# Kernel optimization log

Hardware: AMD Instinct MI355X
Metric: run time of the kernel (lower is better)

Reference implementation:

```python
import jax, jax.numpy as jnp
import numpy as np

NEG_SLOPE = 0.2  # GATConv default negative_slope


def gat_conv(x, row, col, W, b, a_src, a_dst, N):
    # GATConv, heads=1, flow='target_to_source': i=row (central), j=col (neighbor)
    h = x @ W                                                   # [N, C]
    e = jax.nn.leaky_relu((h @ a_src)[col] + (h @ a_dst)[row], NEG_SLOPE)  # [E]
    m = jax.ops.segment_max(e, row, num_segments=N)             # segment softmax over row
    w = jnp.exp(e - m[row])
    denom = jax.ops.segment_sum(w, row, num_segments=N)
    alpha = w / (denom[row] + 1e-16)
    out = jax.ops.segment_sum(alpha[:, None] * h[col], row, num_segments=N)
    return out + b


def lstm_scan(xs_t, Wih, Whh, bih, bhh):
    # xs_t: [L, N, C] -> hidden states [L, N, H]; PyTorch gate order i,f,g,o
    H = Whh.shape[1]
    Nn = xs_t.shape[1]
    bias = bih + bhh
    def step(carry, xt):
        h, c = carry
        g = xt @ Wih.T + h @ Whh.T + bias
        i, f, gg, o = jnp.split(g, 4, axis=-1)
        c = jax.nn.sigmoid(f) * c + jax.nn.sigmoid(i) * jnp.tanh(gg)
        h = jax.nn.sigmoid(o) * jnp.tanh(c)
        return (h, c), h
    init = (jnp.zeros((Nn, H), xs_t.dtype), jnp.zeros((Nn, H), xs_t.dtype))
    _, hs = jax.lax.scan(step, init, xs_t)
    return hs


def jk_lstm(xst, Wih_f, Whh_f, bih_f, bhh_f, Wih_b, Whh_b, bih_b, bhh_b, att_W, att_b):
    # xst: [L, N, C]; bidirectional LSTM over layer dim, attention-weighted sum
    hf = lstm_scan(xst, Wih_f, Whh_f, bih_f, bhh_f)
    hb = lstm_scan(xst[::-1], Wih_b, Whh_b, bih_b, bhh_b)[::-1]
    h = jnp.concatenate([hf, hb], axis=-1)                      # [L, N, 2H]
    score = jnp.einsum('lnh,h->ln', h, att_W) + att_b           # [L, N]
    alpha = jax.nn.softmax(score, axis=0)                       # softmax over layers
    return jnp.einsum('lnc,ln->nc', xst, alpha)                 # [N, C]


def setup_inputs() -> dict:
    key = jax.random.key(0)
    ks = list(jax.random.split(key, 32))
    N, E, C = 50000, 800000, 128
    L = 3
    H = (L * C) // 2  # 192; PyG JumpingKnowledge lstm hidden size
    s = 0.05
    d = {}
    d['x'] = jax.random.normal(ks[0], (N, 3), jnp.float32)
    d['edge_index'] = jax.random.randint(ks[1], (2, E), 0, N, jnp.int64)
    d['gat_W0'] = jax.random.normal(ks[2], (3, C)) * 0.3
    d['gat_b0'] = jnp.zeros((C,))
    d['gat_as0'] = jax.random.normal(ks[3], (C,)) * s
    d['gat_ad0'] = jax.random.normal(ks[4], (C,)) * s
    d['gat_W'] = jax.random.normal(ks[5], (L - 1, C, C)) * s
    d['gat_b'] = jnp.zeros((L - 1, C))
    d['gat_as'] = jax.random.normal(ks[6], (L - 1, C)) * s
    d['gat_ad'] = jax.random.normal(ks[7], (L - 1, C)) * s
    d['lstm_Wih_f'] = jax.random.normal(ks[8], (4 * H, C)) * s
    d['lstm_Whh_f'] = jax.random.normal(ks[9], (4 * H, H)) * s
    d['lstm_bih_f'] = jnp.zeros((4 * H,))
    d['lstm_bhh_f'] = jnp.zeros((4 * H,))
    d['lstm_Wih_b'] = jax.random.normal(ks[10], (4 * H, C)) * s
    d['lstm_Whh_b'] = jax.random.normal(ks[11], (4 * H, H)) * s
    d['lstm_bih_b'] = jnp.zeros((4 * H,))
    d['lstm_bhh_b'] = jnp.zeros((4 * H,))
    d['att_W'] = jax.random.normal(ks[12], (2 * H,)) * s
    d['att_b'] = jnp.zeros((1,))
    d['nW1'] = jax.random.normal(ks[13], (C, C)) * s
    d['nb1'] = jnp.zeros((C,))
    d['nW2'] = jax.random.normal(ks[14], (C, 2)) * s
    d['nb2'] = jnp.zeros((2,))
    d['eW1'] = jax.random.normal(ks[15], (2 * C, C)) * s
    d['eb1'] = jnp.zeros((C,))
    d['eW2'] = jax.random.normal(ks[16], (C, 2)) * s
    d['eb2'] = jnp.zeros((2,))
    return d


def reference(x, edge_index, gat_W0, gat_b0, gat_as0, gat_ad0, gat_W, gat_b, gat_as, gat_ad,
              lstm_Wih_f, lstm_Whh_f, lstm_bih_f, lstm_bhh_f,
              lstm_Wih_b, lstm_Whh_b, lstm_bih_b, lstm_bhh_b,
              att_W, att_b, nW1, nb1, nW2, nb2, eW1, eb1, eW2, eb2):
    N = x.shape[0]
    row, col = edge_index[0], edge_index[1]
    xs = []
    h = jax.nn.relu(gat_conv(x, row, col, gat_W0, gat_b0, gat_as0, gat_ad0, N))
    xs.append(h)
    for l in range(gat_W.shape[0]):  # fixed small layer count
        h = jax.nn.relu(gat_conv(h, row, col, gat_W[l], gat_b[l], gat_as[l], gat_ad[l], N))
        xs.append(h)
    xst = jnp.stack(xs, axis=0)  # [L, N, C]
    h = jk_lstm(xst, lstm_Wih_f, lstm_Whh_f, lstm_bih_f, lstm_bhh_f,
                lstm_Wih_b, lstm_Whh_b, lstm_bih_b, lstm_bhh_b, att_W, att_b)
    # node classifier (dropout is identity in eval)
    node_out = jax.nn.softmax(jax.nn.relu(h @ nW1 + nb1) @ nW2 + nb2, axis=1)
    # edge representation gather + concat, then edge classifier
    edge_rep = jnp.concatenate([h[row], h[col]], axis=1)  # [E, 2C]
    edge_out = jax.nn.softmax(jax.nn.relu(edge_rep @ eW1 + eb1) @ eW2 + eb2, axis=1)
    return node_out, edge_out
```

## Files before the change

### kernel.cpp

```cpp
#include <hip/hip_runtime.h>
#include <cstdint>
#include <cstddef>


#define NIN 28
#define MAXJOBS 20

struct InPtrs { const void* p[NIN]; int n[NIN]; };

struct ConvJobs {
    const void* src[MAXJOBS];
    float* dst[MAXJOBS];
    int n[MAXJOBS];
    int ai[MAXJOBS];
    int blk0[MAXJOBS + 1];
    int njobs;
};

typedef short s16x4 __attribute__((ext_vector_type(4)));
typedef short s16x8 __attribute__((ext_vector_type(8)));
typedef float f32x4 __attribute__((ext_vector_type(4)));
typedef unsigned short u16x8 __attribute__((ext_vector_type(8)));

__device__ __forceinline__ float bf2f(unsigned short v) {
    unsigned int u = ((unsigned int)v) << 16;
    return __uint_as_float(u);
}

__device__ __forceinline__ unsigned short f2bf(float x) {
    unsigned int u = __float_as_uint(x);
    unsigned int r = u + 0x7fffu + ((u >> 16) & 1u);
    return (unsigned short)(r >> 16);
}

__device__ __forceinline__ float rdx(const void* p, size_t i, int isf32) {
    return isf32 ? ((const float*)p)[i] : bf2f(((const unsigned short*)p)[i]);
}

__device__ __forceinline__ float frcp(float x) {
    return __builtin_amdgcn_rcpf(x);
}

__device__ __forceinline__ float sigm(float x) {
    return frcp(1.f + __expf(-x));
}

__device__ __forceinline__ float fast_tanh(float x) {
    return 1.f - 2.f * frcp(__expf(2.f * x) + 1.f);
}

__global__ void k_sniff(InPtrs in, int* flags) {
    int ai = blockIdx.x;
    if (ai >= NIN) return;
    __shared__ int cnt;
    if (threadIdx.x == 0) cnt = 0;
    __syncthreads();
    if (ai == 1) {
        const int* w = (const int*)in.p[1];
        int nw = in.n[1] < 512 ? in.n[1] : 512;
        int local = 0;
        for (int i = threadIdx.x; i < nw; i += blockDim.x)
            if ((i & 1) && w[i] != 0) local++;
        atomicAdd(&cnt, local);
        __syncthreads();
        if (threadIdx.x == 0) flags[1] = (cnt < 4) ? 1 : 0;
        return;
    }
    const unsigned short* u = (const unsigned short*)in.p[ai];
    int ns = in.n[ai] < 256 ? in.n[ai] : 256;
    int local = 0;
    for (int i = threadIdx.x; i < ns; i += blockDim.x) {
        if (i & 1) continue;
        unsigned short v = u[i];
        int e = (v >> 7) & 0xff;
        if ((v & 0x7fff) != 0 && (e < 100 || e > 154)) local++;
    }
    atomicAdd(&cnt, local);
    __syncthreads();
    if (threadIdx.x == 0) flags[ai] = (cnt * 4 >= ns) ? 1 : 0;
}

__global__ void k_convall(ConvJobs J, const int* __restrict__ flags) {
    int b = blockIdx.x;
    int j = 0;
    while (j + 1 < J.njobs && b >= J.blk0[j + 1]) ++j;
    int i = (b - J.blk0[j]) * 256 + threadIdx.x;
    if (i >= J.n[j]) return;
    J.dst[j][i] = rdx(J.src[j], i, flags[J.ai[j]]);
}

__global__ void k_conve(const void* src, int* row, int* col, int* cnt,
                        int E, const int* flags) {
    int i = blockIdx.x * blockDim.x + threadIdx.x;
    if (i >= E) return;
    int r, c;
    if (flags[1]) {
        const long long* s = (const long long*)src;
        r = (int)s[i];
        c = (int)s[(size_t)E + i];
    } else {
        const int* s = (const int*)src;
        r = s[i];
        c = s[(size_t)E + i];
    }
    row[i] = r;
    col[i] = c;
    atomicAdd(&cnt[r], 1);
}

__global__ void k_scan1(const int* __restrict__ deg, int* __restrict__ indptr,
                        int* __restrict__ bsums, int N) {
    __shared__ int buf[1024];
    const int t = threadIdx.x;
    const int base = blockIdx.x * 1024;
    int v = (base + t < N) ? deg[base + t] : 0;
    buf[t] = v;
    __syncthreads();
    for (int ofs = 1; ofs < 1024; ofs <<= 1) {
        int add = (t >= ofs) ? buf[t - ofs] : 0;
        __syncthreads();
        buf[t] += add;
        __syncthreads();
    }
    if (base + t < N) indptr[base + t] = buf[t] - v;
    if (t == 1023) bsums[blockIdx.x] = buf[1023];
}

__global__ void k_scan2(int* bsums, int nb) {
    if (threadIdx.x == 0 && blockIdx.x == 0) {
        int acc = 0;
        for (int j = 0; j < nb; ++j) { int v = bsums[j]; bsums[j] = acc; acc += v; }
        bsums[nb] = acc;
    }
}

__global__ void k_scan3(const int* __restrict__ bsums, int* __restrict__ indptr,
                        int* __restrict__ cnt, int N, int nb) {
    int i = blockIdx.x * blockDim.x + threadIdx.x;
    if (i < N) {
        indptr[i] += bsums[i >> 10];
        cnt[i] = 0;
    }
    if (i == 0) indptr[N] = bsums[nb];
}

__global__ void k_fill(const int* __restrict__ row, const int* __restrict__ col,
                       const int* __restrict__ indptr, int* __restrict__ cur,
                       int* __restrict__ colS, int* __restrict__ eidx, int E) {
    int i = blockIdx.x * blockDim.x + threadIdx.x;
    if (i >= E) return;
    int r = row[i];
    int p = indptr[r] + atomicAdd(&cur[r], 1);
    colS[p] = col[i];
    eidx[p] = i;
}

__global__ __launch_bounds__(256) void k_lin0(
    const float* __restrict__ x, const float* __restrict__ W0,
    const float* __restrict__ asrc, const float* __restrict__ adst,
    unsigned short* __restrict__ hlin, float* __restrict__ hs, float* __restrict__ hd,
    int N) {
    const int wid = threadIdx.x >> 6, lane = threadIdx.x & 63;
    const int n = blockIdx.x * 4 + wid;
    if (n >= N) return;
    float x0 = x[(size_t)n * 3], x1 = x[(size_t)n * 3 + 1], x2 = x[(size_t)n * 3 + 2];
    const int c0 = lane, c1 = lane + 64;
    float h0 = x0 * W0[c0] + x1 * W0[128 + c0] + x2 * W0[256 + c0];
    float h1 = x0 * W0[c1] + x1 * W0[128 + c1] + x2 * W0[256 + c1];
    hlin[(size_t)n * 128 + c0] = f2bf(h0);
    hlin[(size_t)n * 128 + c1] = f2bf(h1);
    float sp = h0 * asrc[c0] + h1 * asrc[c1];
    float dp = h0 * adst[c0] + h1 * adst[c1];
    for (int o = 32; o; o >>= 1) { sp += __shfl_down(sp, o); dp += __shfl_down(dp, o); }
    if (lane == 0) { hs[n] = sp; hd[n] = dp; }
}

__global__ void k_wpackg(const float* __restrict__ Wcanon,
                         unsigned short* __restrict__ Wg) {
    int idx = blockIdx.x * blockDim.x + threadIdx.x;
    if (idx >= 2 * 4 * 8 * 512) return;
    int layer = idx / 16384;
    int r  = idx % 16384;
    int kb = r / 4096;
    int r2 = r % 4096;
    int f  = r2 / 512;
    int q  = r2 % 512;
    int lane = q >> 3, j = q & 7;
    int k   = kb * 32 + ((j >> 2) * 16) + ((lane >> 4) * 4) + (j & 3);
    int col = f * 16 + (lane & 15);
    Wg[idx] = f2bf(Wcanon[(size_t)layer * 16384 + (size_t)k * 128 + col]);
}

__global__ void k_wpackt(const float* __restrict__ nW1, const float* __restrict__ eW1,
                         unsigned short* __restrict__ Wt) {
    int idx = blockIdx.x * blockDim.x + threadIdx.x;
    if (idx >= 4 * 24 * 512) return;
    int kb = idx / (24 * 512);
    int r  = idx % (24 * 512);
    int fr = r / 512;
    int q  = r % 512;
    int lane = q >> 3, j = q & 7;
    int k   = kb * 32 + ((j >> 2) * 16) + ((lane >> 4) * 4) + (j & 3);
    int grp = fr >> 3;
    int col = (fr & 7) * 16 + (lane & 15);
    float v;
    if (grp == 0)      v = nW1[(size_t)k * 128 + col];
    else if (grp == 1) v = eW1[(size_t)k * 128 + col];
    else               v = eW1[(size_t)(128 + k) * 128 + col];
    Wt[idx] = f2bf(v);
}

__global__ __launch_bounds__(512) void k_linm(
    const unsigned short* __restrict__ xin,
    const unsigned short* __restrict__ Wg,
    const float* __restrict__ asrc, const float* __restrict__ adst,
    unsigned short* __restrict__ hlin, float* __restrict__ hs, float* __restrict__ hd,
    int N) {
    __shared__ unsigned short AS[64][136];
    __shared__ float hsS[64], hdS[64];
    const int t = threadIdx.x;
    const int f = t >> 6, lane = t & 63;
    const int n0 = blockIdx.x * 64;
    const int ccol = lane & 15;
    const int klane = lane >> 4;
    const int lrow = klane * 4;
    const int akl = klane * 4;
    const int m = f * 16 + ccol;

    const float asv = asrc[m], adv = adst[m];

    for (int i = t; i < 1024; i += 512) {
        int r = i >> 4, kq = (i & 15) * 8;
        u16x8 v = (u16x8)(0);
        if (n0 + r < N) v = *(const u16x8*)(xin + (size_t)(n0 + r) * 128 + kq);
        *(u16x8*)&AS[r][kq] = v;
    }
    if (t < 64) { hsS[t] = 0.f; hdS[t] = 0.f; }
    __syncthreads();

    f32x4 acc[4];
    #pragma unroll
    for (int rf = 0; rf < 4; ++rf) acc[rf] = (f32x4)(0.f);
    #pragma unroll
    for (int kb = 0; kb < 4; ++kb) {
        s16x8 b = *(const s16x8*)(Wg + ((size_t)kb * 8 + f) * 512 + lane * 8);
        const int k0 = kb * 32 + akl;
        #pragma unroll
        for (int rf = 0; rf < 4; ++rf) {
            s16x4 alo = *(const s16x4*)&AS[rf * 16 + ccol][k0];
            s16x4 ahi = *(const s16x4*)&AS[rf * 16 + ccol][k0 + 16];
            s16x8 av = __builtin_shufflevector(alo, ahi, 0, 1, 2, 3, 4, 5, 6, 7);
            acc[rf] = __builtin_amdgcn_mfma_f32_16x16x32_bf16(av, b, acc[rf], 0, 0, 0);
        }
    }
    __syncthreads();

    float sp[16], dp[16];
    #pragma unroll
    for (int rf = 0; rf < 4; ++rf) {
        #pragma unroll
        for (int reg = 0; reg < 4; ++reg) {
            float h = acc[rf][reg];
            int ci = rf * 4 + reg;
            AS[rf * 16 + lrow + reg][m] = f2bf(h);
            sp[ci] = h * asv;
            dp[ci] = h * adv;
        }
    }
    #pragma unroll
    for (int o = 1; o < 16; o <<= 1) {
        #pragma unroll
        for (int i = 0; i < 16; ++i) { sp[i] += __shfl_xor(sp[i], o); dp[i] += __shfl_xor(dp[i], o); }
    }
    if (ccol == 0) {
        #pragma unroll
        for (int i = 0; i < 16; ++i) {
            int row = (i >> 2) * 16 + lrow + (i & 3);
            atomicAdd(&hsS[row], sp[i]);
            atomicAdd(&hdS[row], dp[i]);
        }
    }
    __syncthreads();

    for (int i = t; i < 1024; i += 512) {
        int r = i >> 4, kq = (i & 15) * 8;
        if (n0 + r < N)
            *(u16x8*)(hlin + (size_t)(n0 + r) * 128 + kq) = *(const u16x8*)&AS[r][kq];
    }
    if (t < 64 && n0 + t < N) { hs[n0 + t] = hsS[t]; hd[n0 + t] = hdS[t]; }
}

__global__ __launch_bounds__(256) void k_aggr(
    const unsigned short* __restrict__ hlin, const float* __restrict__ hs,
    const float* __restrict__ hd,
    const int* __restrict__ indptr, const int* __restrict__ colS,
    const float* __restrict__ b, unsigned short* __restrict__ xout, int N) {
    const int wid = threadIdx.x >> 6, lane = threadIdx.x & 63;
    const int n = blockIdx.x * 4 + wid;
    if (n >= N) return;
    const int s = indptr[n], epos = indptr[n + 1];
    const float hdv = hd[n];
    const int c0 = lane, c1 = lane + 64;
    float m = -1e30f, d = 0.f, a0 = 0.f, a1 = 0.f;
    int idx = s;
    for (; idx + 8 <= epos; idx += 8) {
        int cl[8];
        #pragma unroll
        for (int j = 0; j < 8; ++j) cl[j] = colS[idx + j];
        float e[8];
        #pragma unroll
        for (int j = 0; j < 8; ++j) {
            float ev = hs[cl[j]] + hdv;
            e[j] = (ev > 0.f) ? ev : 0.2f * ev;
        }
        float v0[8], v1[8];
        #pragma unroll
        for (int j = 0; j < 8; ++j) {
            const unsigned short* hp = hlin + (size_t)cl[j] * 128;
            v0[j] = bf2f(hp[c0]);
            v1[j] = bf2f(hp[c1]);
        }
        float m8 = e[0];
        #pragma unroll
        for (int j = 1; j < 8; ++j) m8 = fmaxf(m8, e[j]);
        if (m8 > m) {
            float sc = __expf(m - m8);
            a0 *= sc; a1 *= sc; d *= sc; m = m8;
        }
        #pragma unroll
        for (int j = 0; j < 8; ++j) {
            float w = __expf(e[j] - m);
            a0 += w * v0[j];
            a1 += w * v1[j];
            d  += w;
        }
    }
    for (; idx < epos; ++idx) {
        int col = colS[idx];
        float e = hs[col] + hdv;
        e = (e > 0.f) ? e : 0.2f * e;
        const unsigned short* hr = hlin + (size_t)col * 128;
        float v0 = bf2f(hr[c0]), v1 = bf2f(hr[c1]);
        if (e > m) {
            float sc = __expf(m - e);
            a0 = a0 * sc + v0;
            a1 = a1 * sc + v1;
            d  = d * sc + 1.f;
            m  = e;
        } else {
            float w = __expf(e - m);
            a0 += w * v0;
            a1 += w * v1;
            d  += w;
        }
    }
    float inv = frcp(d + 1e-16f);
    float r0 = a0 * inv + b[c0];
    float r1 = a1 * inv + b[c1];
    xout[(size_t)n * 128 + c0] = f2bf(fmaxf(r0, 0.f));
    xout[(size_t)n * 128 + c1] = f2bf(fmaxf(r1, 0.f));
}

__global__ void k_wpack(const void* Wihf, const void* Whhf,
                        const void* Wihb, const void* Whhb,
                        const void* bihf, const void* bhhf,
                        const void* bihb, const void* bhhb,
                        const int* __restrict__ flags,
                        unsigned short* __restrict__ Bpack, float* __restrict__ bsum) {
    int idx = blockIdx.x * blockDim.x + threadIdx.x;
    const int TOT = 2 * 10 * 48 * 512;
    if (idx < TOT) {
        int dir = idx / (10 * 48 * 512);
        int r   = idx % (10 * 48 * 512);
        int kb  = r / (48 * 512);
        int r2  = r % (48 * 512);
        int f   = r2 / 512;
        int q   = r2 % 512;
        int lane = q >> 3, j = q & 7;
        int k   = kb * 32 + ((j >> 2) * 16) + ((lane >> 4) * 4) + (j & 3);
        int col = f * 16 + (lane & 15);
        float v;
        if (k < 128)
            v = dir ? rdx(Wihb, (size_t)col * 128 + k, flags[14])
                    : rdx(Wihf, (size_t)col * 128 + k, flags[10]);
        else
            v = dir ? rdx(Whhb, (size_t)col * 192 + (k - 128), flags[15])
                    : rdx(Whhf, (size_t)col * 192 + (k - 128), flags[11]);
        Bpack[idx] = f2bf(v);
    }
    if (idx < 2 * 768) {
        int d = idx / 768, j = idx % 768;
        bsum[idx] = d ? rdx(bihb, j, flags[16]) + rdx(bhhb, j, flags[17])
                      : rdx(bihf, j, flags[12]) + rdx(bhhf, j, flags[13]);
    }
}

__global__ __launch_bounds__(768, 3) void k_lstm_mfma(
    const unsigned short* __restrict__ xsb,
    const unsigned short* __restrict__ Bpack,
    const float* __restrict__ bsum,
    const float* __restrict__ attW,
    float* __restrict__ scoreP,
    int N) {
    __shared__ unsigned short AS[64][332];
    __shared__ float scoreS[64];
    const int t = threadIdx.x;
    const int bf = t >> 6, lane = t & 63;
    const int dir = blockIdx.y;
    const int n0 = blockIdx.x * 64;
    const int ccol = lane & 15;
    const int klane = lane >> 4;
    const int lrow = klane * 4;
    const int akl = klane * 4;
    const int m = bf * 16 + ccol;

    const float bI = bsum[dir * 768 + m];
    const float bF = bsum[dir * 768 + 192 + m];
    const float bG = bsum[dir * 768 + 384 + m];
    const float bO = bsum[dir * 768 + 576 + m];
    const float awt = attW[dir * 192 + m];
    float cst[16];
    #pragma unroll
    for (int i = 0; i < 16; ++i) cst[i] = 0.f;

    const unsigned short* Bd = Bpack + (size_t)dir * 10 * 48 * 512;

    for (int s = 0; s < 3; ++s) {
        const int l = dir ? (2 - s) : s;
        {
            const unsigned short* xsrc = xsb + ((size_t)l * N + n0) * 128;
            for (int i = t; i < 1024; i += 768) {
                int r = i >> 4, kq = (i & 15) * 8;
                u16x8 v = (u16x8)(0);
                if (n0 + r < N) v = *(const u16x8*)(xsrc + (size_t)r * 128 + kq);
                *(u16x8*)&AS[r][kq] = v;
            }
        }
        if (t < 64) scoreS[t] = 0.f;
        __syncthreads();

        const int KB = s ? 10 : 4;
        f32x4 acc[4][4];
        #pragma unroll
        for (int rf = 0; rf < 4; ++rf)
            #pragma unroll
            for (int g = 0; g < 4; ++g) acc[rf][g] = (f32x4)(0.f);
        s16x8 bA[4], bB[4];
        {
            const unsigned short* bb = Bd + (size_t)bf * 512 + lane * 8;
            #pragma unroll
            for (int g = 0; g < 4; ++g) bA[g] = *(const s16x8*)(bb + (size_t)g * 6144);
        }
        for (int kb = 0; kb < KB; kb += 2) {
            {
                const unsigned short* bb = Bd + ((size_t)(kb + 1) * 48 + bf) * 512 + lane * 8;
                #pragma unroll
                for (int g = 0; g < 4; ++g) bB[g] = *(const s16x8*)(bb + (size_t)g * 6144);
            }
            {
                const int k0 = kb * 32 + akl;
                s16x8 av[4];
                #pragma unroll
                for (int rf = 0; rf < 4; ++rf) {
                    s16x4 alo = *(const s16x4*)&AS[rf * 16 + ccol][k0];
                    s16x4 ahi = *(const s16x4*)&AS[rf * 16 + ccol][k0 + 16];
                    av[rf] = __builtin_shufflevector(alo, ahi, 0, 1, 2, 3, 4, 5, 6, 7);
                }
                #pragma unroll
                for (int rf = 0; rf < 4; ++rf)
                    #pragma unroll
                    for (int g = 0; g < 4; ++g)
                        acc[rf][g] = __builtin_amdgcn_mfma_f32_16x16x32_bf16(
                            av[rf], bA[g], acc[rf][g], 0, 0, 0);
            }
            if (kb + 2 < KB) {
                const unsigned short* bb = Bd + ((size_t)(kb + 2) * 48 + bf) * 512 + lane * 8;
                #pragma unroll
                for (int g = 0; g < 4; ++g) bA[g] = *(const s16x8*)(bb + (size_t)g * 6144);
            }
            {
                const int k0 = (kb + 1) * 32 + akl;
                s16x8 av[4];
                #pragma unroll
                for (int rf = 0; rf < 4; ++rf) {
                    s16x4 alo = *(const s16x4*)&AS[rf * 16 + ccol][k0];
                    s16x4 ahi = *(const s16x4*)&AS[rf * 16 + ccol][k0 + 16];
                    av[rf] = __builtin_shufflevector(alo, ahi, 0, 1, 2, 3, 4, 5, 6, 7);
                }
                #pragma unroll
                for (int rf = 0; rf < 4; ++rf)
                    #pragma unroll
                    for (int g = 0; g < 4; ++g)
                        acc[rf][g] = __builtin_amdgcn_mfma_f32_16x16x32_bf16(
                            av[rf], bB[g], acc[rf][g], 0, 0, 0);
            }
        }
        __syncthreads();

        float sp[16];
        #pragma unroll
        for (int rf = 0; rf < 4; ++rf) {
            #pragma unroll
            for (int reg = 0; reg < 4; ++reg) {
                float gI = acc[rf][0][reg] + bI;
                float gF = acc[rf][1][reg] + bF;
                float gG = acc[rf][2][reg] + bG;
                float gO = acc[rf][3][reg] + bO;
                float ig = sigm(gI);
                float fg = sigm(gF);
                float gt = fast_tanh(gG);
                float og = sigm(gO);
                int ci = rf * 4 + reg;
                float cn = fg * cst[ci] + ig * gt;
                cst[ci] = cn;
                float hh = og * fast_tanh(cn);
                AS[rf * 16 + lrow + reg][128 + m] = f2bf(hh);
                sp[ci] = hh * awt;
            }
        }
        #pragma unroll
        for (int o = 1; o < 16; o <<= 1) {
            #pragma unroll
            for (int i = 0; i < 16; ++i) sp[i] += __shfl_xor(sp[i], o);
        }
        if (ccol == 0) {
            #pragma unroll
            for (int i = 0; i < 16; ++i)
                atomicAdd(&scoreS[(i >> 2) * 16 + lrow + (i & 3)], sp[i]);
        }
        __syncthreads();
        if (t < 64 && n0 + t < N)
            scoreP[(size_t)(dir * 3 + l) * N + n0 + t] = scoreS[t];
    }
}

__global__ __launch_bounds__(512) void k_tailm(
    const unsigned short* __restrict__ xsb, const float* __restrict__ scoreP,
    const unsigned short* __restrict__ Wt,
    const float* __restrict__ nb1, const float* __restrict__ nW2,
    const float* __restrict__ nb2, const float* __restrict__ eb1,
    unsigned short* __restrict__ P, unsigned short* __restrict__ Q,
    float* __restrict__ out, int N) {
    __shared__ unsigned short AS[64][136];
    __shared__ float al[64][4];
    __shared__ float lgt[64][2];
    const int t = threadIdx.x;
    const int f = t >> 6, lane = t & 63;
    const int n0 = blockIdx.x * 64;
    const int ccol = lane & 15;
    const int klane = lane >> 4;
    const int lrow = klane * 4;
    const int akl = klane * 4;
    const int m = f * 16 + ccol;

    if (t < 64) {
        int n = n0 + t;
        float e0 = 0.f, e1 = 0.f, e2 = 0.f;
        if (n < N) {
            float s0 = scoreP[n]                 + scoreP[(size_t)3 * N + n];
            float s1 = scoreP[(size_t)N + n]     + scoreP[(size_t)4 * N + n];
            float s2 = scoreP[(size_t)2 * N + n] + scoreP[(size_t)5 * N + n];
            float mm = fmaxf(s0, fmaxf(s1, s2));
            e0 = __expf(s0 - mm); e1 = __expf(s1 - mm); e2 = __expf(s2 - mm);
            float inv = frcp(e0 + e1 + e2);
            e0 *= inv; e1 *= inv; e2 *= inv;
        }
        al[t][0] = e0; al[t][1] = e1; al[t][2] = e2;
        lgt[t][0] = 0.f; lgt[t][1] = 0.f;
    }
    __syncthreads();

    const size_t L1o = (size_t)N * 128, L2o = 2 * L1o;
    for (int i = t; i < 1024; i += 512) {
        int r = i >> 4, kq = (i & 15) * 8;
        u16x8 o8 = (u16x8)(0);
        if (n0 + r < N) {
            size_t base = (size_t)(n0 + r) * 128 + kq;
            u16x8 a = *(const u16x8*)(xsb + base);
            u16x8 b = *(const u16x8*)(xsb + L1o + base);
            u16x8 c = *(const u16x8*)(xsb + L2o + base);
            float w0 = al[r][0], w1 = al[r][1], w2 = al[r][2];
            #pragma unroll
            for (int j = 0; j < 8; ++j)
                o8[j] = f2bf(w0 * bf2f(a[j]) + w1 * bf2f(b[j]) + w2 * bf2f(c[j]));
        }
        *(u16x8*)&AS[r][kq] = o8;
    }
    __syncthreads();

    f32x4 accN[4], accP[4], accQ[4];
    #pragma unroll
    for (int rf = 0; rf < 4; ++rf) { accN[rf] = (f32x4)(0.f); accP[rf] = (f32x4)(0.f); accQ[rf] = (f32x4)(0.f); }
    #pragma unroll
    for (int kb = 0; kb < 4; ++kb) {
        s16x8 bN = *(const s16x8*)(Wt + ((size_t)kb * 24 + f) * 512 + lane * 8);
        s16x8 bP = *(const s16x8*)(Wt + ((size_t)kb * 24 + 8 + f) * 512 + lane * 8);
        s16x8 bQ = *(const s16x8*)(Wt + ((size_t)kb * 24 + 16 + f) * 512 + lane * 8);
        const int k0 = kb * 32 + akl;
        #pragma unroll
        for (int rf = 0; rf < 4; ++rf) {
            s16x4 alo = *(const s16x4*)&AS[rf * 16 + ccol][k0];
            s16x4 ahi = *(const s16x4*)&AS[rf * 16 + ccol][k0 + 16];
            s16x8 av = __builtin_shufflevector(alo, ahi, 0, 1, 2, 3, 4, 5, 6, 7);
            accN[rf] = __builtin_amdgcn_mfma_f32_16x16x32_bf16(av, bN, accN[rf], 0, 0, 0);
            accP[rf] = __builtin_amdgcn_mfma_f32_16x16x32_bf16(av, bP, accP[rf], 0, 0, 0);
            accQ[rf] = __builtin_amdgcn_mfma_f32_16x16x32_bf16(av, bQ, accQ[rf], 0, 0, 0);
        }
    }
    __syncthreads();

    {
        const float nb1v = nb1[m];
        const float w20 = nW2[2 * m], w21 = nW2[2 * m + 1];
        float s0[16], s1[16];
        #pragma unroll
        for (int rf = 0; rf < 4; ++rf) {
            #pragma unroll
            for (int reg = 0; reg < 4; ++reg) {
                float h = fmaxf(accN[rf][reg] + nb1v, 0.f);
                int ci = rf * 4 + reg;
                s0[ci] = h * w20;
                s1[ci] = h * w21;
            }
        }
        #pragma unroll
        for (int o = 1; o < 16; o <<= 1) {
            #pragma unroll
            for (int i = 0; i < 16; ++i) { s0[i] += __shfl_xor(s0[i], o); s1[i] += __shfl_xor(s1[i], o); }
        }
        if (ccol == 0) {
            #pragma unroll
            for (int i = 0; i < 16; ++i) {
                int row = (i >> 2) * 16 + lrow + (i & 3);
                atomicAdd(&lgt[row][0], s0[i]);
                atomicAdd(&lgt[row][1], s1[i]);
            }
        }
    }
    {
        const float eb1v = eb1[m];
        #pragma unroll
        for (int rf = 0; rf < 4; ++rf)
            #pragma unroll
            for (int reg = 0; reg < 4; ++reg)
                AS[rf * 16 + lrow + reg][m] = f2bf(accP[rf][reg] + eb1v);
    }
    __syncthreads();
    if (t < 64 && n0 + t < N) {
        float l0 = lgt[t][0] + nb2[0], l1 = lgt[t][1] + nb2[1];
        float mm = fmaxf(l0, l1);
        float e0 = __expf(l0 - mm), e1 = __expf(l1 - mm);
        float inv = frcp(e0 + e1);
        out[2 * (size_t)(n0 + t)]     = e0 * inv;
        out[2 * (size_t)(n0 + t) + 1] = e1 * inv;
    }
    for (int i = t; i < 1024; i += 512) {
        int r = i >> 4, kq = (i & 15) * 8;
        if (n0 + r < N)
            *(u16x8*)(P + (size_t)(n0 + r) * 128 + kq) = *(const u16x8*)&AS[r][kq];
    }
    __syncthreads();
    #pragma unroll
    for (int rf = 0; rf < 4; ++rf)
        #pragma unroll
        for (int reg = 0; reg < 4; ++reg)
            AS[rf * 16 + lrow + reg][m] = f2bf(accQ[rf][reg]);
    __syncthreads();
    for (int i = t; i < 1024; i += 512) {
        int r = i >> 4, kq = (i & 15) * 8;
        if (n0 + r < N)
            *(u16x8*)(Q + (size_t)(n0 + r) * 128 + kq) = *(const u16x8*)&AS[r][kq];
    }
}

__global__ __launch_bounds__(256) void k_edge3(
    const unsigned short* __restrict__ P, const unsigned short* __restrict__ Q,
    const int* __restrict__ indptr, const int* __restrict__ colS,
    const int* __restrict__ eidx,
    const float* __restrict__ W2, const float* __restrict__ b2,
    float* __restrict__ out, int N) {
    const int wid = threadIdx.x >> 6, lane = threadIdx.x & 63;
    const int n = blockIdx.x * 4 + wid;
    if (n >= N) return;
    const int sl = lane & 15, g = lane >> 4;
    const int s = indptr[n], e = indptr[n + 1];
    float pf[8];
    {
        u16x8 pv = *(const u16x8*)(P + (size_t)n * 128 + sl * 8);
        #pragma unroll
        for (int j = 0; j < 8; ++j) pf[j] = bf2f(pv[j]);
    }
    const float* W2f = W2;
    const float b20 = b2[0], b21 = b2[1];
    for (int p = s + g; p < e; p += 8) {
        int p1 = p + 4;
        bool v1 = p1 < e;
        int col0 = colS[p],  eo0 = eidx[p];
        int col1 = v1 ? colS[p1] : col0;
        int eo1  = v1 ? eidx[p1] : 0;
        u16x8 qv0 = *(const u16x8*)(Q + (size_t)col0 * 128 + sl * 8);
        u16x8 qv1 = *(const u16x8*)(Q + (size_t)col1 * 128 + sl * 8);
        float l00 = 0.f, l01 = 0.f, l10 = 0.f, l11 = 0.f;
        #pragma unroll
        for (int j = 0; j < 8; ++j) {
            int ch = sl * 8 + j;
            float wA = W2f[ch * 2], wB = W2f[ch * 2 + 1];
            float h0 = fmaxf(pf[j] + bf2f(qv0[j]), 0.f);
            float h1 = fmaxf(pf[j] + bf2f(qv1[j]), 0.f);
            l00 += h0 * wA; l01 += h0 * wB;
            l10 += h1 * wA; l11 += h1 * wB;
        }
        #pragma unroll
        for (int o = 1; o < 16; o <<= 1) {
            l00 += __shfl_xor(l00, o); l01 += __shfl_xor(l01, o);
            l10 += __shfl_xor(l10, o); l11 += __shfl_xor(l11, o);
        }
        if (sl == 0) {
            {
                float a = l00 + b20, b = l01 + b21;
                float mm = fmaxf(a, b);
                float e0 = __expf(a - mm), e1 = __expf(b - mm);
                float inv = frcp(e0 + e1);
                out[2 * (size_t)N + 2 * (size_t)eo0]     = e0 * inv;
                out[2 * (size_t)N + 2 * (size_t)eo0 + 1] = e1 * inv;
            }
            if (v1) {
                float a = l10 + b20, b = l11 + b21;
                float mm = fmaxf(a, b);
                float e0 = __expf(a - mm), e1 = __expf(b - mm);
                float inv = frcp(e0 + e1);
                out[2 * (size_t)N + 2 * (size_t)eo1]     = e0 * inv;
                out[2 * (size_t)N + 2 * (size_t)eo1 + 1] = e1 * inv;
            }
        }
    }
}

extern "C" void kernel_launch(void* const* d_in, const int* in_sizes, int n_in,
                              void* d_out, int out_size, void* d_ws, size_t ws_size,
                              hipStream_t stream) {
    if (n_in < NIN) return;
    const int N = in_sizes[0] / 3;
    const int E = in_sizes[1] / 2;

    char* ws = (char*)d_ws;
    size_t off = 0;
    auto alloc = [&](size_t bytes) -> char* {
        char* p = ws + off;
        off = (off + bytes + 255) & ~(size_t)255;
        return p;
    };
    int* flags = (int*)alloc(32 * sizeof(int));
    int* bsums = (int*)alloc(128 * sizeof(int));
    float* canon[NIN];
    for (int i = 0; i < NIN; ++i) canon[i] = nullptr;
    for (int i = 0; i < NIN; ++i) {
        if (i == 1 || (i >= 10 && i <= 17)) continue;
        canon[i] = (float*)alloc((size_t)in_sizes[i] * 4);
    }
    int* row32  = (int*)alloc((size_t)E * 4);
    int* col32  = (int*)alloc((size_t)E * 4);
    int* indptr = (int*)alloc((size_t)(N + 1) * 4);
    int* cnt    = (int*)alloc((size_t)N * 4);
    int* colS   = (int*)alloc((size_t)E * 4);
    int* eidx   = (int*)alloc((size_t)E * 4);
    float* hs   = (float*)alloc((size_t)N * 4);
    float* hd   = (float*)alloc((size_t)N * 4);
    float* hJK  = (float*)alloc((size_t)N * 128 * 4);
    unsigned short* hlin = (unsigned short*)hJK;
    unsigned short* xsb = (unsigned short*)alloc((size_t)3 * N * 128 * 2);
    unsigned short* Bpack = (unsigned short*)alloc((size_t)2 * 10 * 48 * 512 * 2);
    unsigned short* Wg = (unsigned short*)alloc((size_t)2 * 4 * 8 * 512 * 2);
    unsigned short* Wt = (unsigned short*)alloc((size_t)4 * 24 * 512 * 2);
    float* bsum = (float*)alloc((size_t)2 * 768 * 4);
    float* scoreP = (float*)alloc((size_t)6 * N * 4);
    if (off > ws_size) return;
    unsigned short* P = (unsigned short*)hJK;
    unsigned short* Q = (unsigned short*)hJK + (size_t)N * 128;

    InPtrs ip;
    for (int i = 0; i < NIN; ++i) { ip.p[i] = d_in[i]; ip.n[i] = in_sizes[i]; }

    k_sniff<<<NIN, 256, 0, stream>>>(ip, flags);

    {
        ConvJobs J;
        int nj = 0, blk = 0;
        for (int i = 0; i < NIN; ++i) {
            if (i == 1 || (i >= 10 && i <= 17)) continue;
            J.src[nj] = d_in[i];
            J.dst[nj] = canon[i];
            J.n[nj] = in_sizes[i];
            J.ai[nj] = i;
            J.blk0[nj] = blk;
            blk += (in_sizes[i] + 255) / 256;
            ++nj;
        }
        J.blk0[nj] = blk;
        J.njobs = nj;
        k_convall<<<blk, 256, 0, stream>>>(J, flags);
    }
    hipMemsetAsync(cnt, 0, (size_t)N * 4, stream);
    k_conve<<<(E + 255) / 256, 256, 0, stream>>>(d_in[1], row32, col32, cnt, E, flags);
    k_wpack<<<(2 * 10 * 48 * 512 + 255) / 256, 256, 0, stream>>>(
        d_in[10], d_in[11], d_in[14], d_in[15],
        d_in[12], d_in[13], d_in[16], d_in[17], flags, Bpack, bsum);
    k_wpackg<<<(2 * 4 * 8 * 512 + 255) / 256, 256, 0, stream>>>(canon[6], Wg);
    k_wpackt<<<(4 * 24 * 512 + 255) / 256, 256, 0, stream>>>(canon[20], canon[24], Wt);

    const int nb1k = (N + 1023) / 1024;
    k_scan1<<<nb1k, 1024, 0, stream>>>(cnt, indptr, bsums, N);
    k_scan2<<<1, 64, 0, stream>>>(bsums, nb1k);
    k_scan3<<<(N + 255) / 256, 256, 0, stream>>>(bsums, indptr, cnt, N, nb1k);
    k_fill<<<(E + 255) / 256, 256, 0, stream>>>(row32, col32, indptr, cnt, colS, eidx, E);

    k_lin0<<<(N + 3) / 4, 256, 0, stream>>>(canon[0], canon[2], canon[4], canon[5],
                                            hlin, hs, hd, N);
    k_aggr<<<(N + 3) / 4, 256, 0, stream>>>(hlin, hs, hd, indptr, colS, canon[3], xsb, N);
    for (int l = 1; l < 3; ++l) {
        const unsigned short* Wgl = Wg + (size_t)(l - 1) * 4 * 8 * 512;
        const float* bb = canon[7] + (size_t)(l - 1) * 128;
        const float* as = canon[8] + (size_t)(l - 1) * 128;
        const float* ad = canon[9] + (size_t)(l - 1) * 128;
        k_linm<<<(N + 63) / 64, 512, 0, stream>>>(xsb + (size_t)(l - 1) * N * 128, Wgl,
                                                  as, ad, hlin, hs, hd, N);
        k_aggr<<<(N + 3) / 4, 256, 0, stream>>>(hlin, hs, hd, indptr, colS, bb,
                                                xsb + (size_t)l * N * 128, N);
    }

    dim3 lgrid((N + 63) / 64, 2);
    k_lstm_mfma<<<lgrid, 768, 0, stream>>>(xsb, Bpack, bsum, canon[18], scoreP, N);

    float* out = (float*)d_out;
    k_tailm<<<(N + 63) / 64, 512, 0, stream>>>(xsb, scoreP, Wt,
                                               canon[21], canon[22], canon[23], canon[25],
                                               P, Q, out, N);
    k_edge3<<<(N + 3) / 4, 256, 0, stream>>>(P, Q, indptr, colS, eidx,
                                             canon[26], canon[27], out, N);
}
```

Before: 594.9 us.

## Fuse preprocessing kernels into one launch and prefetch next LSTM layer input

Merges the input conversion, edge conversion/degree count, and three weight-packing kernels into a single multi-role k_prep launch. Weight packing now reads the raw inputs directly, so the canonical float copies of those weights are no longer made. Inside the LSTM MFMA kernel, the next layer's input tile is loaded into registers during the current step's score computation and written to shared memory afterward, removing a barrier-separated load phase. This cuts launch overhead and hides load latency, at the cost of extra registers and a larger kernel-argument struct.

```diff
diff --git a/kernel.cpp b/kernel.cpp
--- a/kernel.cpp
+++ b/kernel.cpp
@@ -8,13 +8,19 @@
 
 struct InPtrs { const void* p[NIN]; int n[NIN]; };
 
-struct ConvJobs {
+struct PrepCfg {
     const void* src[MAXJOBS];
     float* dst[MAXJOBS];
     int n[MAXJOBS];
     int ai[MAXJOBS];
     int blk0[MAXJOBS + 1];
     int njobs;
+    int cvB, wB, gB, tB;
+    const void* esrc; int* row; int* col; int* cnt; int E;
+    const void *Wihf, *Whhf, *Wihb, *Whhb, *bihf, *bhhf, *bihb, *bhhb;
+    unsigned short* Bpack; float* bsum;
+    const void* Wgsrc; unsigned short* Wg;
+    const void* nW1src; const void* eW1src; unsigned short* Wt;
 };
 
 typedef short s16x4 __attribute__((ext_vector_type(4)));
@@ -80,32 +86,96 @@
     if (threadIdx.x == 0) flags[ai] = (cnt * 4 >= ns) ? 1 : 0;
 }
 
-__global__ void k_convall(ConvJobs J, const int* __restrict__ flags) {
-    int b = blockIdx.x;
-    int j = 0;
-    while (j + 1 < J.njobs && b >= J.blk0[j + 1]) ++j;
-    int i = (b - J.blk0[j]) * 256 + threadIdx.x;
-    if (i >= J.n[j]) return;
-    J.dst[j][i] = rdx(J.src[j], i, flags[J.ai[j]]);
-}
-
-__global__ void k_conve(const void* src, int* row, int* col, int* cnt,
-                        int E, const int* flags) {
-    int i = blockIdx.x * blockDim.x + threadIdx.x;
-    if (i >= E) return;
-    int r, c;
-    if (flags[1]) {
-        const long long* s = (const long long*)src;
-        r = (int)s[i];
-        c = (int)s[(size_t)E + i];
-    } else {
-        const int* s = (const int*)src;
-        r = s[i];
-        c = s[(size_t)E + i];
-    }
-    row[i] = r;
-    col[i] = c;
-    atomicAdd(&cnt[r], 1);
+__global__ void k_prep(PrepCfg C, const int* __restrict__ flags) {
+    const int b = blockIdx.x;
+    const int tid = threadIdx.x;
+    if (b < C.cvB) {
+        int j = 0;
+        while (j + 1 < C.njobs && b >= C.blk0[j + 1]) ++j;
+        int i = (b - C.blk0[j]) * 256 + tid;
+        if (i < C.n[j]) C.dst[j][i] = rdx(C.src[j], i, flags[C.ai[j]]);
+        return;
+    }
+    if (b < C.wB) {
+        int i = (b - C.cvB) * 256 + tid;
+        if (i >= C.E) return;
+        int r, c;
+        if (flags[1]) {
+            const long long* s = (const long long*)C.esrc;
+            r = (int)s[i];
+            c = (int)s[(size_t)C.E + i];
+        } else {
+            const int* s = (const int*)C.esrc;
+            r = s[i];
+            c = s[(size_t)C.E + i];
+        }
+        C.row[i] = r;
+        C.col[i] = c;
+        atomicAdd(&C.cnt[r], 1);
+        return;
+    }
+    if (b < C.gB) {
+        int idx = (b - C.wB) * 256 + tid;
+        const int TOT = 2 * 10 * 48 * 512;
+        if (idx < TOT) {
+            int dir = idx / (10 * 48 * 512);
+            int r   = idx % (10 * 48 * 512);
+            int kb  = r / (48 * 512);
+            int r2  = r % (48 * 512);
+            int f   = r2 / 512;
+            int q   = r2 % 512;
+            int lane = q >> 3, j = q & 7;
+            int k   = kb * 32 + ((j >> 2) * 16) + ((lane >> 4) * 4) + (j & 3);
+            int col = f * 16 + (lane & 15);
+            float v;
+            if (k < 128)
+                v = dir ? rdx(C.Wihb, (size_t)col * 128 + k, flags[14])
+                        : rdx(C.Wihf, (size_t)col * 128 + k, flags[10]);
+            else
+                v = dir ? rdx(C.Whhb, (size_t)col * 192 + (k - 128), flags[15])
+                        : rdx(C.Whhf, (size_t)col * 192 + (k - 128), flags[11]);
+            C.Bpack[idx] = f2bf(v);
+        }
+        if (idx < 2 * 768) {
+            int d = idx / 768, j = idx % 768;
+            C.bsum[idx] = d ? rdx(C.bihb, j, flags[16]) + rdx(C.bhhb, j, flags[17])
+                            : rdx(C.bihf, j, flags[12]) + rdx(C.bhhf, j, flags[13]);
+        }
+        return;
+    }
+    if (b < C.tB) {
+        int idx = (b - C.gB) * 256 + tid;
+        if (idx >= 2 * 4 * 8 * 512) return;
+        int layer = idx / 16384;
+        int r  = idx % 16384;
+        int kb = r / 4096;
+        int r2 = r % 4096;
+        int f  = r2 / 512;
+        int q  = r2 % 512;
+        int lane = q >> 3, j = q & 7;
+        int k   = kb * 32 + ((j >> 2) * 16) + ((lane >> 4) * 4) + (j & 3);
+        int col = f * 16 + (lane & 15);
+        C.Wg[idx] = f2bf(rdx(C.Wgsrc, (size_t)layer * 16384 + (size_t)k * 128 + col,
+                             flags[6]));
+        return;
+    }
+    {
+        int idx = (b - C.tB) * 256 + tid;
+        if (idx >= 4 * 24 * 512) return;
+        int kb = idx / (24 * 512);
+        int r  = idx % (24 * 512);
+        int fr = r / 512;
+        int q  = r % 512;
+        int lane = q >> 3, j = q & 7;
+        int k   = kb * 32 + ((j >> 2) * 16) + ((lane >> 4) * 4) + (j & 3);
+        int grp = fr >> 3;
+        int col = (fr & 7) * 16 + (lane & 15);
+        float v;
+        if (grp == 0)      v = rdx(C.nW1src, (size_t)k * 128 + col, flags[20]);
+        else if (grp == 1) v = rdx(C.eW1src, (size_t)k * 128 + col, flags[24]);
+        else               v = rdx(C.eW1src, (size_t)(128 + k) * 128 + col, flags[24]);
+        C.Wt[idx] = f2bf(v);
+    }
 }
 
 __global__ void k_scan1(const int* __restrict__ deg, int* __restrict__ indptr,
@@ -175,41 +245,6 @@
     if (lane == 0) { hs[n] = sp; hd[n] = dp; }
 }
 
-__global__ void k_wpackg(const float* __restrict__ Wcanon,
-                         unsigned short* __restrict__ Wg) {
-    int idx = blockIdx.x * blockDim.x + threadIdx.x;
-    if (idx >= 2 * 4 * 8 * 512) return;
-    int layer = idx / 16384;
-    int r  = idx % 16384;
-    int kb = r / 4096;
-    int r2 = r % 4096;
-    int f  = r2 / 512;
-    int q  = r2 % 512;
-    int lane = q >> 3, j = q & 7;
-    int k   = kb * 32 + ((j >> 2) * 16) + ((lane >> 4) * 4) + (j & 3);
-    int col = f * 16 + (lane & 15);
-    Wg[idx] = f2bf(Wcanon[(size_t)layer * 16384 + (size_t)k * 128 + col]);
-}
-
-__global__ void k_wpackt(const float* __restrict__ nW1, const float* __restrict__ eW1,
-                         unsigned short* __restrict__ Wt) {
-    int idx = blockIdx.x * blockDim.x + threadIdx.x;
-    if (idx >= 4 * 24 * 512) return;
-    int kb = idx / (24 * 512);
-    int r  = idx % (24 * 512);
-    int fr = r / 512;
-    int q  = r % 512;
-    int lane = q >> 3, j = q & 7;
-    int k   = kb * 32 + ((j >> 2) * 16) + ((lane >> 4) * 4) + (j & 3);
-    int grp = fr >> 3;
-    int col = (fr & 7) * 16 + (lane & 15);
-    float v;
-    if (grp == 0)      v = nW1[(size_t)k * 128 + col];
-    else if (grp == 1) v = eW1[(size_t)k * 128 + col];
-    else               v = eW1[(size_t)(128 + k) * 128 + col];
-    Wt[idx] = f2bf(v);
-}
-
 __global__ __launch_bounds__(512) void k_linm(
     const unsigned short* __restrict__ xin,
     const unsigned short* __restrict__ Wg,
@@ -359,40 +394,6 @@
     float r1 = a1 * inv + b[c1];
     xout[(size_t)n * 128 + c0] = f2bf(fmaxf(r0, 0.f));
     xout[(size_t)n * 128 + c1] = f2bf(fmaxf(r1, 0.f));
-}
-
-__global__ void k_wpack(const void* Wihf, const void* Whhf,
-                        const void* Wihb, const void* Whhb,
-                        const void* bihf, const void* bhhf,
-                        const void* bihb, const void* bhhb,
-                        const int* __restrict__ flags,
-                        unsigned short* __restrict__ Bpack, float* __restrict__ bsum) {
-    int idx = blockIdx.x * blockDim.x + threadIdx.x;
-    const int TOT = 2 * 10 * 48 * 512;
-    if (idx < TOT) {
-        int dir = idx / (10 * 48 * 512);
-        int r   = idx % (10 * 48 * 512);
-        int kb  = r / (48 * 512);
-        int r2  = r % (48 * 512);
-        int f   = r2 / 512;
-        int q   = r2 % 512;
-        int lane = q >> 3, j = q & 7;
-        int k   = kb * 32 + ((j >> 2) * 16) + ((lane >> 4) * 4) + (j & 3);
-        int col = f * 16 + (lane & 15);
-        float v;
-        if (k < 128)
-            v = dir ? rdx(Wihb, (size_t)col * 128 + k, flags[14])
-                    : rdx(Wihf, (size_t)col * 128 + k, flags[10]);
-        else
-            v = dir ? rdx(Whhb, (size_t)col * 192 + (k - 128), flags[15])
-                    : rdx(Whhf, (size_t)col * 192 + (k - 128), flags[11]);
-        Bpack[idx] = f2bf(v);
-    }
-    if (idx < 2 * 768) {
-        int d = idx / 768, j = idx % 768;
-        bsum[idx] = d ? rdx(bihb, j, flags[16]) + rdx(bhhb, j, flags[17])
-                      : rdx(bihf, j, flags[12]) + rdx(bhhf, j, flags[13]);
-    }
 }
 
 __global__ __launch_bounds__(768, 3) void k_lstm_mfma(
@@ -425,19 +426,21 @@
 
     const unsigned short* Bd = Bpack + (size_t)dir * 10 * 48 * 512;
 
+    {
+        const int l0 = dir ? 2 : 0;
+        const unsigned short* xsrc = xsb + ((size_t)l0 * N + n0) * 128;
+        for (int i = t; i < 1024; i += 768) {
+            int r = i >> 4, kq = (i & 15) * 8;
+            u16x8 v = (u16x8)(0);
+            if (n0 + r < N) v = *(const u16x8*)(xsrc + (size_t)r * 128 + kq);
+            *(u16x8*)&AS[r][kq] = v;
+        }
+    }
+    if (t < 64) scoreS[t] = 0.f;
+    __syncthreads();
+
     for (int s = 0; s < 3; ++s) {
         const int l = dir ? (2 - s) : s;
-        {
-            const unsigned short* xsrc = xsb + ((size_t)l * N + n0) * 128;
-            for (int i = t; i < 1024; i += 768) {
-                int r = i >> 4, kq = (i & 15) * 8;
-                u16x8 v = (u16x8)(0);
-                if (n0 + r < N) v = *(const u16x8*)(xsrc + (size_t)r * 128 + kq);
-                *(u16x8*)&AS[r][kq] = v;
-            }
-        }
-        if (t < 64) scoreS[t] = 0.f;
-        __syncthreads();
 
         const int KB = s ? 10 : 4;
         f32x4 acc[4][4];
@@ -497,6 +500,20 @@
         }
         __syncthreads();
 
+        u16x8 nx0 = (u16x8)(0), nx1 = (u16x8)(0);
+        if (s < 2) {
+            const int ln = dir ? (1 - s) : (s + 1);
+            const unsigned short* xsrc = xsb + ((size_t)ln * N + n0) * 128;
+            {
+                int r = t >> 4, kq = (t & 15) * 8;
+                if (n0 + r < N) nx0 = *(const u16x8*)(xsrc + (size_t)r * 128 + kq);
+            }
+            if (t < 256) {
+                int i = t + 768, r = i >> 4, kq = (i & 15) * 8;
+                if (n0 + r < N) nx1 = *(const u16x8*)(xsrc + (size_t)r * 128 + kq);
+            }
+        }
+
         float sp[16];
         #pragma unroll
         for (int rf = 0; rf < 4; ++rf) {
@@ -528,9 +545,24 @@
             for (int i = 0; i < 16; ++i)
                 atomicAdd(&scoreS[(i >> 2) * 16 + lrow + (i & 3)], sp[i]);
         }
+
+        if (s < 2) {
+            {
+                int r = t >> 4, kq = (t & 15) * 8;
+                *(u16x8*)&AS[r][kq] = nx0;
+            }
+            if (t < 256) {
+                int i = t + 768, r = i >> 4, kq = (i & 15) * 8;
+                *(u16x8*)&AS[r][kq] = nx1;
+            }
+        }
         __syncthreads();
-        if (t < 64 && n0 + t < N)
-            scoreP[(size_t)(dir * 3 + l) * N + n0 + t] = scoreS[t];
+
+        if (t < 64) {
+            if (n0 + t < N)
+                scoreP[(size_t)(dir * 3 + l) * N + n0 + t] = scoreS[t];
+            scoreS[t] = 0.f;
+        }
     }
 }
 
@@ -750,12 +782,15 @@
         off = (off + bytes + 255) & ~(size_t)255;
         return p;
     };
+    auto skipCanon = [](int i) {
+        return i == 1 || (i >= 10 && i <= 17) || i == 6 || i == 20 || i == 24;
+    };
     int* flags = (int*)alloc(32 * sizeof(int));
     int* bsums = (int*)alloc(128 * sizeof(int));
     float* canon[NIN];
     for (int i = 0; i < NIN; ++i) canon[i] = nullptr;
     for (int i = 0; i < NIN; ++i) {
-        if (i == 1 || (i >= 10 && i <= 17)) continue;
+        if (skipCanon(i)) continue;
         canon[i] = (float*)alloc((size_t)in_sizes[i] * 4);
     }
     int* row32  = (int*)alloc((size_t)E * 4);
@@ -783,30 +818,35 @@
 
     k_sniff<<<NIN, 256, 0, stream>>>(ip, flags);
 
+    hipMemsetAsync(cnt, 0, (size_t)N * 4, stream);
     {
-        ConvJobs J;
+        PrepCfg C;
         int nj = 0, blk = 0;
         for (int i = 0; i < NIN; ++i) {
-            if (i == 1 || (i >= 10 && i <= 17)) continue;
-            J.src[nj] = d_in[i];
-            J.dst[nj] = canon[i];
-            J.n[nj] = in_sizes[i];
-            J.ai[nj] = i;
-            J.blk0[nj] = blk;
+            if (skipCanon(i)) continue;
+            C.src[nj] = d_in[i];
+            C.dst[nj] = canon[i];
+            C.n[nj] = in_sizes[i];
+            C.ai[nj] = i;
+            C.blk0[nj] = blk;
             blk += (in_sizes[i] + 255) / 256;
             ++nj;
         }
-        J.blk0[nj] = blk;
-        J.njobs = nj;
-        k_convall<<<blk, 256, 0, stream>>>(J, flags);
-    }
-    hipMemsetAsync(cnt, 0, (size_t)N * 4, stream);
-    k_conve<<<(E + 255) / 256, 256, 0, stream>>>(d_in[1], row32, col32, cnt, E, flags);
-    k_wpack<<<(2 * 10 * 48 * 512 + 255) / 256, 256, 0, stream>>>(
-        d_in[10], d_in[11], d_in[14], d_in[15],
-        d_in[12], d_in[13], d_in[16], d_in[17], flags, Bpack, bsum);
-    k_wpackg<<<(2 * 4 * 8 * 512 + 255) / 256, 256, 0, stream>>>(canon[6], Wg);
-    k_wpackt<<<(4 * 24 * 512 + 255) / 256, 256, 0, stream>>>(canon[20], canon[24], Wt);
+        C.blk0[nj] = blk;
+        C.njobs = nj;
+        C.cvB = blk;
+        blk += (E + 255) / 256;                      C.wB = blk;
+        blk += (2 * 10 * 48 * 512 + 255) / 256;      C.gB = blk;
+        blk += (2 * 4 * 8 * 512 + 255) / 256;        C.tB = blk;
+        blk += (4 * 24 * 512 + 255) / 256;
+        C.esrc = d_in[1]; C.row = row32; C.col = col32; C.cnt = cnt; C.E = E;
+        C.Wihf = d_in[10]; C.Whhf = d_in[11]; C.Wihb = d_in[14]; C.Whhb = d_in[15];
+        C.bihf = d_in[12]; C.bhhf = d_in[13]; C.bihb = d_in[16]; C.bhhb = d_in[17];
+        C.Bpack = Bpack; C.bsum = bsum;
+        C.Wgsrc = d_in[6]; C.Wg = Wg;
+        C.nW1src = d_in[20]; C.eW1src = d_in[24]; C.Wt = Wt;
+        k_prep<<<blk, 256, 0, stream>>>(C, flags);
+    }
 
     const int nb1k = (N + 1023) / 1024;
     k_scan1<<<nb1k, 1024, 0, stream>>>(cnt, indptr, bsums, N);
```

Measured after the change: 584.7 us. No clear change (-1.7%).
